# Kernel tuning notes

Hardware: AMD Instinct MI355X
Metric: run time of the kernel (lower is better)

## Reference

```python
import jax, jax.numpy as jnp
import numpy as np
from jax import lax

B, T, H, Q = 32, 2000, 896, 256
SUB = H // 2


def wavrnn_normalize(x):
    return 2.0 * x / 255.0 - 1.0


def setup_inputs() -> dict:
    key = jax.random.key(0)
    ks = jax.random.split(key, 10)
    p = lambda k, shape: (jax.random.normal(k, shape, dtype=jnp.float32) * 0.02)
    return {
        "sample": jax.random.randint(ks[0], (B, T, 2), 0, 256, dtype=jnp.int32),
        "cts": jax.random.randint(ks[1], (B, T, 1), 0, 256, dtype=jnp.int32),
        "state": jnp.zeros((B, H), dtype=jnp.float32),
        "R": p(ks[2], (3 * H, H)),
        "Wc": p(ks[3], (3 * SUB, 2)),
        "Wf": p(ks[4], (3 * SUB, 3)),
        "b_u": jnp.zeros((H,), jnp.float32),
        "b_r": jnp.zeros((H,), jnp.float32),
        "b_e": jnp.zeros((H,), jnp.float32),
        "Wc1": p(ks[5], (SUB, SUB)),
        "bc1": jnp.zeros((SUB,), jnp.float32),
        "Wc2": p(ks[6], (Q, SUB)),
        "bc2": jnp.zeros((Q,), jnp.float32),
        "Wf1": p(ks[7], (SUB, SUB)),
        "bf1": jnp.zeros((SUB,), jnp.float32),
        "Wf2": p(ks[8], (Q, SUB)),
        "bf2": jnp.zeros((Q,), jnp.float32),
    }


def reference(sample, cts, state, R, Wc, Wf, b_u, b_r, b_e,
              Wc1, bc1, Wc2, bc2, Wf1, bf1, Wf2, bf2):
    s = wavrnn_normalize(sample.astype(jnp.float32))          # [B,T,2]
    c = wavrnn_normalize(cts.astype(jnp.float32))             # [B,T,1]
    s_f = jnp.concatenate([s, c], axis=2)                     # [B,T,3]

    proj_c = jnp.einsum('btk,ok->bto', s, Wc)                 # [B,T,3*SUB]
    proj_f = jnp.einsum('btk,ok->bto', s_f, Wf)               # [B,T,3*SUB]
    utc, rtc, etc_ = jnp.split(proj_c, 3, axis=2)
    utf, rtf, etf = jnp.split(proj_f, 3, axis=2)
    fwd_u = jnp.concatenate([utc, utf], axis=2)               # [B,T,H]
    fwd_r = jnp.concatenate([rtc, rtf], axis=2)
    fwd_e = jnp.concatenate([etc_, etf], axis=2)

    # time-major for scan: [T,B,H]
    xs = (jnp.swapaxes(fwd_u, 0, 1), jnp.swapaxes(fwd_r, 0, 1), jnp.swapaxes(fwd_e, 0, 1))

    def step(h, x):
        fu, fr, fe = x                                        # each [B,H]
        r_ = h @ R.T                                          # [B,3H]
        r_u, r_r, r_e = jnp.split(r_, 3, axis=1)
        ut = jax.nn.sigmoid(r_u + fu + b_u)
        rt = jax.nn.sigmoid(r_r + fr + b_r)
        et = jnp.tanh(rt * r_e + fe + b_e)
        h_new = ut * h + (1.0 - ut) * et
        return h_new, h_new

    last, states = lax.scan(step, state, xs)                  # states [T,B,H]
    states = jnp.swapaxes(states, 0, 1)                       # [B,T,H]
    htc, htf = jnp.split(states, 2, axis=2)                   # [B,T,SUB] each

    ct = jax.nn.log_softmax(
        jax.nn.relu(jnp.einsum('btk,ok->bto', htc, Wc1) + bc1) @ Wc2.T + bc2, axis=2)
    ft = jax.nn.log_softmax(
        jax.nn.relu(jnp.einsum('btk,ok->bto', htf, Wf1) + bf1) @ Wf2.T + bf2, axis=2)
    return (ct, ft, last[:, None, :])
```

## Files before the change

### kernel.cpp

```cpp
#include <hip/hip_runtime.h>
#include <hip/hip_bf16.h>

#define B_   32
#define T_   2000
#define H_   896
#define SUB_ 448
#define Q_   256

#define FT_OFF   16384000
#define LAST_OFF 32768000

#define NBLK_ 28

#define WS_FLAGS  0
#define WS_H0     8192
#define WS_WB     65536
#define WS_STATES 1327104

#define WB_W1C 0
#define WB_W1F 200704
#define WB_W2C 401408
#define WB_W2F 516096
#define WB_N   630784

#define SLOT_B 57344
#define SLOT_E 28672

typedef __attribute__((ext_vector_type(8)))  short bf16x8;
typedef __attribute__((ext_vector_type(16))) float f32x16;

__device__ __forceinline__ unsigned short f2bf(float f) {
    unsigned int u = __builtin_bit_cast(unsigned int, f);
    u += 0x7fff + ((u >> 16) & 1);
    return (unsigned short)(u >> 16);
}
__device__ __forceinline__ float bf2f(unsigned short u) {
    return __builtin_bit_cast(float, (unsigned int)u << 16);
}
__device__ __forceinline__ void gload_lds16(const void* g, void* l) {
    __builtin_amdgcn_global_load_lds(
        (const __attribute__((address_space(1))) unsigned int*)g,
        (__attribute__((address_space(3))) unsigned int*)l, 16, 0, 0);
}
__device__ __forceinline__ bf16x8 mk8(short4 a, short4 b) {
    bf16x8 f;
    f[0]=a.x; f[1]=a.y; f[2]=a.z; f[3]=a.w;
    f[4]=b.x; f[5]=b.y; f[6]=b.z; f[7]=b.w;
    return f;
}
__device__ __forceinline__ float fsig(float x) {
    return __builtin_amdgcn_rcpf(1.0f + __expf(-x));
}
__device__ __forceinline__ float ftanh(float x) {
    float xc = fminf(fmaxf(x, -9.0f), 9.0f);
    float z  = __expf(2.0f * xc);
    return 1.0f - 2.0f * __builtin_amdgcn_rcpf(z + 1.0f);
}

__global__ void wavrnn_prep(const float* __restrict__ state,
                            const float* __restrict__ Wc1, const float* __restrict__ Wf1,
                            const float* __restrict__ Wc2, const float* __restrict__ Wf2,
                            unsigned short* __restrict__ wb,
                            unsigned short* __restrict__ h0,
                            int* __restrict__ flags) {
    const int i = blockIdx.x * 256 + threadIdx.x;
    if (i < WB_N) {
        float v;
        if      (i < WB_W1F) v = Wc1[i];
        else if (i < WB_W2C) v = Wf1[i - WB_W1F];
        else if (i < WB_W2F) v = Wc2[i - WB_W2C];
        else                 v = Wf2[i - WB_W2F];
        wb[i] = f2bf(v);
    }
    if (i < 1792) flags[i] = 0;
    if (i < B_ * H_) h0[i] = f2bf(state[i]);
}

__global__ __launch_bounds__(192, 1)
void wavrnn_scan5(const int* __restrict__ sample, const int* __restrict__ cts,
                  const float* __restrict__ state, const float* __restrict__ R,
                  const float* __restrict__ Wc, const float* __restrict__ Wf,
                  const float* __restrict__ b_u, const float* __restrict__ b_r,
                  const float* __restrict__ b_e,
                  const unsigned short* __restrict__ h0,
                  int* __restrict__ flags,
                  unsigned short* __restrict__ states,
                  float* __restrict__ out)
{
    const int tid  = (int)threadIdx.x;
    const int w    = tid >> 6;
    const int lane = tid & 63;
    const int s31  = lane & 31;
    const int hi   = lane >> 5;
    const int b    = (int)blockIdx.x;

    __shared__ __align__(16) char Abuf[32 * 2048];
    __shared__ float gate_out[3][32][34];

    const int jgB = b * 32 + s31;
    bf16x8 Bf[56];
    {
        const float* Rrow = R + (size_t)(w * H_ + jgB) * H_;
        #pragma unroll
        for (int c = 0; c < 56; ++c) {
            const float4 p0 = *(const float4*)(Rrow + 16*c + 4*hi);
            const float4 p1 = *(const float4*)(Rrow + 16*c + 8 + 4*hi);
            bf16x8 f;
            f[0]=(short)f2bf(p0.x); f[1]=(short)f2bf(p0.y);
            f[2]=(short)f2bf(p0.z); f[3]=(short)f2bf(p0.w);
            f[4]=(short)f2bf(p1.x); f[5]=(short)f2bf(p1.y);
            f[6]=(short)f2bf(p1.z); f[7]=(short)f2bf(p1.w);
            Bf[c] = f;
        }
    }

    const int jp  = tid & 15;
    const int sg  = (tid >> 4) & 7;
    const int j0  = 2 * jp;
    const int jg0 = b * 32 + j0;
    float wu[2][3], wr[2][3], we[2][3], gb[2][3];
    float hreg[4][2];
    if (tid < 128) {
        #pragma unroll
        for (int jj = 0; jj < 2; ++jj) {
            const int jg = jg0 + jj;
            if (jg < SUB_) {
                wu[jj][0]=Wc[2*jg];            wu[jj][1]=Wc[2*jg+1];            wu[jj][2]=0.f;
                wr[jj][0]=Wc[2*(SUB_+jg)];     wr[jj][1]=Wc[2*(SUB_+jg)+1];     wr[jj][2]=0.f;
                we[jj][0]=Wc[2*(2*SUB_+jg)];   we[jj][1]=Wc[2*(2*SUB_+jg)+1];   we[jj][2]=0.f;
            } else {
                const int jf = jg - SUB_;
                wu[jj][0]=Wf[3*jf];            wu[jj][1]=Wf[3*jf+1];            wu[jj][2]=Wf[3*jf+2];
                wr[jj][0]=Wf[3*(SUB_+jf)];     wr[jj][1]=Wf[3*(SUB_+jf)+1];     wr[jj][2]=Wf[3*(SUB_+jf)+2];
                we[jj][0]=Wf[3*(2*SUB_+jf)];   we[jj][1]=Wf[3*(2*SUB_+jf)+1];   we[jj][2]=Wf[3*(2*SUB_+jf)+2];
            }
            gb[jj][0]=b_u[jg]; gb[jj][1]=b_r[jg]; gb[jj][2]=b_e[jg];
        }
        #pragma unroll
        for (int q = 0; q < 4; ++q) {
            const int s = sg*4 + q;
            hreg[q][0] = state[(size_t)s*H_ + jg0];
            hreg[q][1] = state[(size_t)s*H_ + jg0 + 1];
        }
    }

    const int v16l = lane * 16;
    const char* abb = Abuf + s31*2048 + 8*s31 + 8*hi;

    #pragma unroll 1
    for (int t = 1; t <= T_; ++t) {
        float s0n[4], s1n[4], c0n[4];
        if (tid < 128) {
            const float kn = 2.0f / 255.0f;
            #pragma unroll
            for (int q = 0; q < 4; ++q) {
                const size_t idx = (size_t)(sg*4 + q)*T_ + (size_t)(t - 1);
                const int2 sv = *(const int2*)(sample + idx*2);
                s0n[q] = kn*(float)sv.x - 1.0f;
                s1n[q] = kn*(float)sv.y - 1.0f;
                c0n[q] = kn*(float)cts[idx] - 1.0f;
            }
        }
        if (w == 0) {
            for (;;) {
                int v = (lane < 2*NBLK_)
                    ? __hip_atomic_load(&flags[lane*32], __ATOMIC_RELAXED, __HIP_MEMORY_SCOPE_AGENT)
                    : 0x7fffffff;
                if (__all(v >= t - 1)) break;
                __builtin_amdgcn_s_sleep(1);
            }
        }
        asm volatile("" ::: "memory");
        __builtin_amdgcn_sched_barrier(0);
        __syncthreads();

        {
            const char* sb = (t == 1) ? (const char*)h0
                                      : (const char*)states + (size_t)(t - 2)*SLOT_B;
            #pragma unroll
            for (int ii = 0; ii < 22; ++ii) {
                const int i = w + 3*ii;
                if (i < 64) {
                    const int sp   = i >> 1;
                    const int half = i & 1;
                    gload_lds16(sb + sp*1784 + half*1024 + v16l,
                                Abuf + sp*2048 + half*1024);
                }
            }
        }
        __syncthreads();

        f32x16 acc0, acc1;
        #pragma unroll
        for (int e = 0; e < 16; ++e) { acc0[e] = 0.0f; acc1[e] = 0.0f; }
        #pragma unroll
        for (int c2 = 0; c2 < 28; ++c2) {
            {
                const short4 p0 = *(const short4*)(abb + 64*c2);
                const short4 p1 = *(const short4*)(abb + 64*c2 + 16);
                acc0 = __builtin_amdgcn_mfma_f32_32x32x16_bf16(mk8(p0, p1), Bf[2*c2], acc0, 0, 0, 0);
            }
            {
                const short4 p0 = *(const short4*)(abb + 64*c2 + 32);
                const short4 p1 = *(const short4*)(abb + 64*c2 + 48);
                acc1 = __builtin_amdgcn_mfma_f32_32x32x16_bf16(mk8(p0, p1), Bf[2*c2+1], acc1, 0, 0, 0);
            }
        }
        #pragma unroll
        for (int e = 0; e < 16; ++e) {
            const int srow = (e & 3) + 8*(e >> 2) + 4*hi;
            gate_out[w][srow][s31] = acc0[e] + acc1[e];
        }
        __syncthreads();

        if (tid < 128) {
            #pragma unroll
            for (int q = 0; q < 4; ++q) {
                const int s = sg*4 + q;
                const float2 g0 = *(const float2*)&gate_out[0][s][j0];
                const float2 g1 = *(const float2*)&gate_out[1][s][j0];
                const float2 g2 = *(const float2*)&gate_out[2][s][j0];
                unsigned int packed = 0;
                #pragma unroll
                for (int jj = 0; jj < 2; ++jj) {
                    const float ru = jj ? g0.y : g0.x;
                    const float rr = jj ? g1.y : g1.x;
                    const float re = jj ? g2.y : g2.x;
                    const float fu = s0n[q]*wu[jj][0] + s1n[q]*wu[jj][1] + c0n[q]*wu[jj][2];
                    const float fr = s0n[q]*wr[jj][0] + s1n[q]*wr[jj][1] + c0n[q]*wr[jj][2];
                    const float fe = s0n[q]*we[jj][0] + s1n[q]*we[jj][1] + c0n[q]*we[jj][2];
                    const float ut = fsig(ru + fu + gb[jj][0]);
                    const float rt = fsig(rr + fr + gb[jj][1]);
                    const float et = ftanh(rt*re + fe + gb[jj][2]);
                    const float hn = ut*hreg[q][jj] + (1.0f - ut)*et;
                    hreg[q][jj] = hn;
                    packed |= (unsigned int)f2bf(hn) << (16*jj);
                    if (t == T_) out[LAST_OFF + (size_t)s*H_ + jg0 + jj] = hn;
                }
                __hip_atomic_store(
                    (unsigned int*)(states + (size_t)(t-1)*SLOT_E + s*H_ + jg0),
                    packed, __ATOMIC_RELAXED, __HIP_MEMORY_SCOPE_AGENT);
            }
        }
        if (w < 2) {
            asm volatile("s_waitcnt vmcnt(0)" ::: "memory");
            if (lane == 0)
                __hip_atomic_store(&flags[(2*b + w)*32], t,
                                   __ATOMIC_RELAXED, __HIP_MEMORY_SCOPE_AGENT);
        }
    }
}

__global__ __launch_bounds__(256, 1)
void wavrnn_head3(const unsigned short* __restrict__ states,
                  const unsigned short* __restrict__ wb,
                  const float* __restrict__ bc1, const float* __restrict__ bc2,
                  const float* __restrict__ bf1, const float* __restrict__ bf2,
                  float* __restrict__ out)
{
    __shared__ __align__(16) char stL[32 * 1920];
    __shared__ __align__(16) char a1L[32 * 1920];

    const int tid  = (int)threadIdx.x;
    const int w    = tid >> 6;
    const int lane = tid & 63;
    const int nl   = lane & 31;
    const int hi   = lane >> 5;
    const int row0 = (int)blockIdx.x * 32;

    #pragma unroll
    for (int ii = 0; ii < 28; ++ii) {
        const int idx = ii*256 + tid;
        const int rp  = idx / 224;
        const int p   = idx - rp*224;
        const int r   = row0 + rp;
        const int sr  = r / 2000;
        const int tr  = r - sr*2000;
        const uint2 v = *(const uint2*)(states + (size_t)tr*SLOT_E + sr*H_ + p*4);
        *(uint2*)(stL + rp*1920 + 8*(rp & 15) + p*8) = v;
    }
    __syncthreads();

    {
        const char* apb = stL + nl*1920 + 8*(nl & 15) + 8*hi;
        #pragma unroll 1
        for (int tt = 0; tt < 7; ++tt) {
            const int nt   = tt*4 + w;
            const int head = nt >= 14;
            const int jt   = nt - head*14;
            const int orow = jt*32 + nl;
            const unsigned short* wrp = wb + (head ? WB_W1F : WB_W1C) + (size_t)orow*448;
            const float bias = (head ? bf1 : bc1)[orow];
            const int ko = head * 896;
            f32x16 acc;
            #pragma unroll
            for (int e = 0; e < 16; ++e) acc[e] = bias;
            #pragma unroll
            for (int c = 0; c < 28; ++c) {
                const short4 a0 = *(const short4*)(apb + ko + 32*c);
                const short4 a1 = *(const short4*)(apb + ko + 32*c + 16);
                const short4 b0 = *(const short4*)((const char*)wrp + 32*c + 8*hi);
                const short4 b1 = *(const short4*)((const char*)wrp + 32*c + 8*hi + 16);
                acc = __builtin_amdgcn_mfma_f32_32x32x16_bf16(mk8(a0, a1), mk8(b0, b1), acc, 0, 0, 0);
            }
            const int jg = head*448 + jt*32 + nl;
            #pragma unroll
            for (int e = 0; e < 16; ++e) {
                const int m2 = (e & 3) + 8*(e >> 2) + 4*hi;
                *(unsigned short*)(a1L + m2*1920 + 8*(m2 & 15) + 2*jg) =
                    f2bf(fmaxf(acc[e], 0.0f));
            }
        }
    }
    __syncthreads();

    {
        unsigned short* lg = (unsigned short*)stL;
        const char* apb = a1L + nl*1920 + 8*(nl & 15) + 8*hi;
        #pragma unroll 1
        for (int tt = 0; tt < 4; ++tt) {
            const int nt   = tt*4 + w;
            const int head = nt >= 8;
            const int ct   = (nt & 7)*32 + nl;
            const unsigned short* wrp = wb + (head ? WB_W2F : WB_W2C) + (size_t)ct*448;
            const float bias = (head ? bf2 : bc2)[ct];
            const int ko = head * 896;
            f32x16 acc;
            #pragma unroll
            for (int e = 0; e < 16; ++e) acc[e] = bias;
            #pragma unroll
            for (int c = 0; c < 28; ++c) {
                const short4 a0 = *(const short4*)(apb + ko + 32*c);
                const short4 a1 = *(const short4*)(apb + ko + 32*c + 16);
                const short4 b0 = *(const short4*)((const char*)wrp + 32*c + 8*hi);
                const short4 b1 = *(const short4*)((const char*)wrp + 32*c + 8*hi + 16);
                acc = __builtin_amdgcn_mfma_f32_32x32x16_bf16(mk8(a0, a1), mk8(b0, b1), acc, 0, 0, 0);
            }
            #pragma unroll
            for (int e = 0; e < 16; ++e) {
                const int m2 = (e & 3) + 8*(e >> 2) + 4*hi;
                lg[m2*520 + head*256 + (nt & 7)*32 + nl] = f2bf(acc[e]);
            }
        }
    }
    __syncthreads();

    {
        const unsigned short* lg = (const unsigned short*)stL;
        #pragma unroll 1
        for (int p = w; p < 64; p += 4) {
            const int hh = p >> 5;
            const int rr = p & 31;
            const ushort4 lv = *(const ushort4*)(lg + rr*520 + hh*256 + 4*lane);
            const float v0 = bf2f(lv.x), v1 = bf2f(lv.y), v2 = bf2f(lv.z), v3 = bf2f(lv.w);
            float m = fmaxf(fmaxf(v0, v1), fmaxf(v2, v3));
            #pragma unroll
            for (int d = 1; d < 64; d <<= 1) m = fmaxf(m, __shfl_xor(m, d));
            float sm = __expf(v0-m) + __expf(v1-m) + __expf(v2-m) + __expf(v3-m);
            #pragma unroll
            for (int d = 1; d < 64; d <<= 1) sm += __shfl_xor(sm, d);
            const float ls = m + __logf(sm);
            float* o = out + (hh ? (size_t)FT_OFF : (size_t)0) + (size_t)(row0 + rr)*Q_ + 4*lane;
            o[0] = v0 - ls; o[1] = v1 - ls; o[2] = v2 - ls; o[3] = v3 - ls;
        }
    }
}

extern "C" void kernel_launch(void* const* d_in, const int* in_sizes, int n_in,
                              void* d_out, int out_size, void* d_ws, size_t ws_size,
                              hipStream_t stream) {
    (void)in_sizes; (void)n_in; (void)out_size; (void)ws_size;
    const int*   sample = (const int*)d_in[0];
    const int*   cts    = (const int*)d_in[1];
    const float* state  = (const float*)d_in[2];
    const float* R      = (const float*)d_in[3];
    const float* Wc     = (const float*)d_in[4];
    const float* Wf     = (const float*)d_in[5];
    const float* b_u    = (const float*)d_in[6];
    const float* b_r    = (const float*)d_in[7];
    const float* b_e    = (const float*)d_in[8];
    const float* Wc1    = (const float*)d_in[9];
    const float* bc1    = (const float*)d_in[10];
    const float* Wc2    = (const float*)d_in[11];
    const float* bc2    = (const float*)d_in[12];
    const float* Wf1    = (const float*)d_in[13];
    const float* bf1    = (const float*)d_in[14];
    const float* Wf2    = (const float*)d_in[15];
    const float* bf2    = (const float*)d_in[16];

    float* out = (float*)d_out;
    int*            flags  = (int*)((char*)d_ws + WS_FLAGS);
    unsigned short* h0     = (unsigned short*)((char*)d_ws + WS_H0);
    unsigned short* wb     = (unsigned short*)((char*)d_ws + WS_WB);
    unsigned short* states = (unsigned short*)((char*)d_ws + WS_STATES);

    wavrnn_prep<<<2464, 256, 0, stream>>>(state, Wc1, Wf1, Wc2, Wf2, wb, h0, flags);
    wavrnn_scan5<<<NBLK_, 192, 0, stream>>>(sample, cts, state, R, Wc, Wf,
                                            b_u, b_r, b_e, h0, flags, states, out);
    wavrnn_head3<<<(B_ * T_) / 32, 256, 0, stream>>>(states, wb, bc1, bc2, bf1, bf2, out);
}
```

Measured before the change: 11.26 ms.

## Halve scan blocks to 14 with 6 waves each and split state load

The persistent GRU scan now runs on 14 blocks of 384 threads instead of 28 blocks of 192. Each block owns 64 hidden columns, with two waves per gate, so fewer blocks have to reach the cross-block flag barrier at every timestep. The per-step load of the previous hidden state into LDS is split into two halves, and the MFMA work on the first half starts while the second half is still loading. Each block now does more per-step work serially, and an extra __syncthreads is added per step.

```diff
diff --git a/kernel.cpp b/kernel.cpp
--- a/kernel.cpp
+++ b/kernel.cpp
@@ -10,7 +10,8 @@
 #define FT_OFF   16384000
 #define LAST_OFF 32768000
 
-#define NBLK_ 28
+#define NBLK_  14
+#define NFLAG_ 56
 
 #define WS_FLAGS  0
 #define WS_H0     8192
@@ -76,8 +77,8 @@
     if (i < B_ * H_) h0[i] = f2bf(state[i]);
 }
 
-__global__ __launch_bounds__(192, 1)
-void wavrnn_scan5(const int* __restrict__ sample, const int* __restrict__ cts,
+__global__ __launch_bounds__(384, 2)
+void wavrnn_scan6(const int* __restrict__ sample, const int* __restrict__ cts,
                   const float* __restrict__ state, const float* __restrict__ R,
                   const float* __restrict__ Wc, const float* __restrict__ Wf,
                   const float* __restrict__ b_u, const float* __restrict__ b_r,
@@ -93,14 +94,16 @@
     const int s31  = lane & 31;
     const int hi   = lane >> 5;
     const int b    = (int)blockIdx.x;
+    const int g    = w >> 1;
+    const int q    = w & 1;
 
     __shared__ __align__(16) char Abuf[32 * 2048];
-    __shared__ float gate_out[3][32][34];
-
-    const int jgB = b * 32 + s31;
+    __shared__ float gate_out[3][32][72];
+
+    const int jgB = b * 64 + q * 32 + s31;
     bf16x8 Bf[56];
     {
-        const float* Rrow = R + (size_t)(w * H_ + jgB) * H_;
+        const float* Rrow = R + (size_t)(g * H_ + jgB) * H_;
         #pragma unroll
         for (int c = 0; c < 56; ++c) {
             const float4 p0 = *(const float4*)(Rrow + 16*c + 4*hi);
@@ -114,13 +117,13 @@
         }
     }
 
-    const int jp  = tid & 15;
-    const int sg  = (tid >> 4) & 7;
+    const int jp  = tid & 31;
+    const int sg  = (tid >> 5) & 7;
     const int j0  = 2 * jp;
-    const int jg0 = b * 32 + j0;
+    const int jg0 = b * 64 + j0;
     float wu[2][3], wr[2][3], we[2][3], gb[2][3];
     float hreg[4][2];
-    if (tid < 128) {
+    if (tid < 256) {
         #pragma unroll
         for (int jj = 0; jj < 2; ++jj) {
             const int jg = jg0 + jj;
@@ -137,10 +140,10 @@
             gb[jj][0]=b_u[jg]; gb[jj][1]=b_r[jg]; gb[jj][2]=b_e[jg];
         }
         #pragma unroll
-        for (int q = 0; q < 4; ++q) {
-            const int s = sg*4 + q;
-            hreg[q][0] = state[(size_t)s*H_ + jg0];
-            hreg[q][1] = state[(size_t)s*H_ + jg0 + 1];
+        for (int qq = 0; qq < 4; ++qq) {
+            const int s = sg*4 + qq;
+            hreg[qq][0] = state[(size_t)s*H_ + jg0];
+            hreg[qq][1] = state[(size_t)s*H_ + jg0 + 1];
         }
     }
 
@@ -150,20 +153,20 @@
     #pragma unroll 1
     for (int t = 1; t <= T_; ++t) {
         float s0n[4], s1n[4], c0n[4];
-        if (tid < 128) {
+        if (tid < 256) {
             const float kn = 2.0f / 255.0f;
             #pragma unroll
-            for (int q = 0; q < 4; ++q) {
-                const size_t idx = (size_t)(sg*4 + q)*T_ + (size_t)(t - 1);
+            for (int qq = 0; qq < 4; ++qq) {
+                const size_t idx = (size_t)(sg*4 + qq)*T_ + (size_t)(t - 1);
                 const int2 sv = *(const int2*)(sample + idx*2);
-                s0n[q] = kn*(float)sv.x - 1.0f;
-                s1n[q] = kn*(float)sv.y - 1.0f;
-                c0n[q] = kn*(float)cts[idx] - 1.0f;
+                s0n[qq] = kn*(float)sv.x - 1.0f;
+                s1n[qq] = kn*(float)sv.y - 1.0f;
+                c0n[qq] = kn*(float)cts[idx] - 1.0f;
             }
         }
         if (w == 0) {
             for (;;) {
-                int v = (lane < 2*NBLK_)
+                int v = (lane < NFLAG_)
                     ? __hip_atomic_load(&flags[lane*32], __ATOMIC_RELAXED, __HIP_MEMORY_SCOPE_AGENT)
                     : 0x7fffffff;
                 if (__all(v >= t - 1)) break;
@@ -174,27 +177,29 @@
         __builtin_amdgcn_sched_barrier(0);
         __syncthreads();
 
-        {
-            const char* sb = (t == 1) ? (const char*)h0
-                                      : (const char*)states + (size_t)(t - 2)*SLOT_B;
-            #pragma unroll
-            for (int ii = 0; ii < 22; ++ii) {
-                const int i = w + 3*ii;
-                if (i < 64) {
-                    const int sp   = i >> 1;
-                    const int half = i & 1;
-                    gload_lds16(sb + sp*1784 + half*1024 + v16l,
-                                Abuf + sp*2048 + half*1024);
-                }
-            }
+        const char* sb = (t == 1) ? (const char*)h0
+                                  : (const char*)states + (size_t)(t - 2)*SLOT_B;
+
+        #pragma unroll
+        for (int ii = 0; ii < 6; ++ii) {
+            const int i = w + 6*ii;
+            if (i < 32)
+                gload_lds16(sb + i*1784 + v16l, Abuf + i*2048);
         }
         __syncthreads();
 
+        #pragma unroll
+        for (int ii = 0; ii < 6; ++ii) {
+            const int i = w + 6*ii;
+            if (i < 32)
+                gload_lds16(sb + i*1784 + 1024 + v16l, Abuf + i*2048 + 1024);
+        }
+
         f32x16 acc0, acc1;
         #pragma unroll
         for (int e = 0; e < 16; ++e) { acc0[e] = 0.0f; acc1[e] = 0.0f; }
         #pragma unroll
-        for (int c2 = 0; c2 < 28; ++c2) {
+        for (int c2 = 0; c2 < 16; ++c2) {
             {
                 const short4 p0 = *(const short4*)(abb + 64*c2);
                 const short4 p1 = *(const short4*)(abb + 64*c2 + 16);
@@ -206,17 +211,32 @@
                 acc1 = __builtin_amdgcn_mfma_f32_32x32x16_bf16(mk8(p0, p1), Bf[2*c2+1], acc1, 0, 0, 0);
             }
         }
+        __syncthreads();
+
+        #pragma unroll
+        for (int c2 = 16; c2 < 28; ++c2) {
+            {
+                const short4 p0 = *(const short4*)(abb + 64*c2);
+                const short4 p1 = *(const short4*)(abb + 64*c2 + 16);
+                acc0 = __builtin_amdgcn_mfma_f32_32x32x16_bf16(mk8(p0, p1), Bf[2*c2], acc0, 0, 0, 0);
+            }
+            {
+                const short4 p0 = *(const short4*)(abb + 64*c2 + 32);
+                const short4 p1 = *(const short4*)(abb + 64*c2 + 48);
+                acc1 = __builtin_amdgcn_mfma_f32_32x32x16_bf16(mk8(p0, p1), Bf[2*c2+1], acc1, 0, 0, 0);
+            }
+        }
         #pragma unroll
         for (int e = 0; e < 16; ++e) {
             const int srow = (e & 3) + 8*(e >> 2) + 4*hi;
-            gate_out[w][srow][s31] = acc0[e] + acc1[e];
+            gate_out[g][srow][q*32 + s31] = acc0[e] + acc1[e];
         }
         __syncthreads();
 
-        if (tid < 128) {
-            #pragma unroll
-            for (int q = 0; q < 4; ++q) {
-                const int s = sg*4 + q;
+        if (tid < 256) {
+            #pragma unroll
+            for (int qq = 0; qq < 4; ++qq) {
+                const int s = sg*4 + qq;
                 const float2 g0 = *(const float2*)&gate_out[0][s][j0];
                 const float2 g1 = *(const float2*)&gate_out[1][s][j0];
                 const float2 g2 = *(const float2*)&gate_out[2][s][j0];
@@ -226,14 +246,14 @@
                     const float ru = jj ? g0.y : g0.x;
                     const float rr = jj ? g1.y : g1.x;
                     const float re = jj ? g2.y : g2.x;
-                    const float fu = s0n[q]*wu[jj][0] + s1n[q]*wu[jj][1] + c0n[q]*wu[jj][2];
-                    const float fr = s0n[q]*wr[jj][0] + s1n[q]*wr[jj][1] + c0n[q]*wr[jj][2];
-                    const float fe = s0n[q]*we[jj][0] + s1n[q]*we[jj][1] + c0n[q]*we[jj][2];
+                    const float fu = s0n[qq]*wu[jj][0] + s1n[qq]*wu[jj][1] + c0n[qq]*wu[jj][2];
+                    const float fr = s0n[qq]*wr[jj][0] + s1n[qq]*wr[jj][1] + c0n[qq]*wr[jj][2];
+                    const float fe = s0n[qq]*we[jj][0] + s1n[qq]*we[jj][1] + c0n[qq]*we[jj][2];
                     const float ut = fsig(ru + fu + gb[jj][0]);
                     const float rt = fsig(rr + fr + gb[jj][1]);
                     const float et = ftanh(rt*re + fe + gb[jj][2]);
-                    const float hn = ut*hreg[q][jj] + (1.0f - ut)*et;
-                    hreg[q][jj] = hn;
+                    const float hn = ut*hreg[qq][jj] + (1.0f - ut)*et;
+                    hreg[qq][jj] = hn;
                     packed |= (unsigned int)f2bf(hn) << (16*jj);
                     if (t == T_) out[LAST_OFF + (size_t)s*H_ + jg0 + jj] = hn;
                 }
@@ -242,10 +262,10 @@
                     packed, __ATOMIC_RELAXED, __HIP_MEMORY_SCOPE_AGENT);
             }
         }
-        if (w < 2) {
+        if (w < 4) {
             asm volatile("s_waitcnt vmcnt(0)" ::: "memory");
             if (lane == 0)
-                __hip_atomic_store(&flags[(2*b + w)*32], t,
+                __hip_atomic_store(&flags[(4*b + w)*32], t,
                                    __ATOMIC_RELAXED, __HIP_MEMORY_SCOPE_AGENT);
         }
     }
@@ -395,7 +415,7 @@
     unsigned short* states = (unsigned short*)((char*)d_ws + WS_STATES);
 
     wavrnn_prep<<<2464, 256, 0, stream>>>(state, Wc1, Wf1, Wc2, Wf2, wb, h0, flags);
-    wavrnn_scan5<<<NBLK_, 192, 0, stream>>>(sample, cts, state, R, Wc, Wf,
+    wavrnn_scan6<<<NBLK_, 384, 0, stream>>>(sample, cts, state, R, Wc, Wf,
                                             b_u, b_r, b_e, h0, flags, states, out);
     wavrnn_head3<<<(B_ * T_) / 32, 256, 0, stream>>>(states, wb, bc1, bc2, bf1, bf2, out);
 }
```

Measured after the change: 21.10 ms. 1.87x slower.
